# Optimization experiments

Hardware: AMD Instinct MI355X
Metric: run time of the kernel (lower is better)

## Reference

```python
import jax, jax.numpy as jnp
import numpy as np

B, P, K, D, T = 512, 64, 8, 512, 50000


def setup_inputs() -> dict:
    key = jax.random.key(0)
    k1, k2, k3, k4, k5, k6 = jax.random.split(key, 6)
    return {
        "inputs": jax.random.normal(k1, (B, P, D), dtype=jnp.float32),
        "title_emb_mat": jax.random.normal(k2, (T, D), dtype=jnp.float32),
        "nbr_batch": jax.random.randint(k3, (B, P, K), 0, B, dtype=jnp.int32),
        "nbr_job": jax.random.randint(k4, (B, P, K), 0, P, dtype=jnp.int32),
        "nbr_title": jax.random.randint(k5, (B, P, K), 0, T, dtype=jnp.int32),
        "nbr_mask": jax.random.randint(k6, (B, P, K), 0, 2, dtype=jnp.int32),
    }


def reference(inputs, title_emb_mat, nbr_batch, nbr_job, nbr_title, nbr_mask):
    # inputs:        [B, P, D]  job embeddings per employee position
    # title_emb_mat: [T, Dt]    title embedding table (Dt == D here)
    # nbr_*:         [B, P, K]  padded metapath neighbor indices + validity mask
    mask = nbr_mask.astype(bool)                              # [B,P,K]
    ref_embs = inputs[nbr_batch, nbr_job]                     # [B,P,K,D] gather of neighbor job embs
    # attention logits: focal emb vs neighbor embs (raw inner product, exp-normalized)
    raw_s = jnp.einsum('bpd,bpkd->bpk', inputs, ref_embs)     # [B,P,K]
    logits = jnp.where(mask, raw_s, jnp.float32(-1e9))
    sim = jax.nn.softmax(logits, axis=-1) * mask              # exact zeros on padded slots;
    # an all-masked (i,pos) -> uniform softmax * 0 mask == 0 row (matches torch 'continue' -> zeros)
    ref_t_embs = title_emb_mat[nbr_title]                     # [B,P,K,Dt] gather of target-title embs
    graph_concat = jnp.einsum('bpk,bpkt->bpt', sim, ref_t_embs)  # [B,P,Dt]
    out = jnp.concatenate([inputs, graph_concat], axis=-1)    # [B,P,D+Dt]
    return out.reshape(B * P, D + title_emb_mat.shape[1])     # torch.cat over batch, axis=0
```

## Files before the change

kernel.cpp:

```cpp
#include <hip/hip_runtime.h>

#define BB 512
#define PP 64
#define KK 8
#define DD 512

typedef float v4f __attribute__((ext_vector_type(4)));

__global__ __launch_bounds__(256, 2) void han_meta_kernel(
    const float* __restrict__ inputs,
    const float* __restrict__ title,
    const int*   __restrict__ nbr_batch,
    const int*   __restrict__ nbr_job,
    const int*   __restrict__ nbr_title,
    const int*   __restrict__ nbr_mask,
    float*       __restrict__ out)
{
    const int lane = threadIdx.x & 63;
    const int row = __builtin_amdgcn_readfirstlane(
        blockIdx.x * 4 + (threadIdx.x >> 6));

    const int* nb = nbr_batch + row * KK;
    const int* nj = nbr_job   + row * KK;
    const int* nt = nbr_title + row * KK;
    const int* nm = nbr_mask  + row * KK;
    int nbk[KK], njk[KK], ntk[KK], nmk[KK];
    #pragma unroll
    for (int k = 0; k < KK; ++k) {
        nbk[k] = __builtin_amdgcn_readfirstlane(nb[k]);
        njk[k] = __builtin_amdgcn_readfirstlane(nj[k]);
        ntk[k] = __builtin_amdgcn_readfirstlane(nt[k]);
        nmk[k] = __builtin_amdgcn_readfirstlane(nm[k]);
    }

    const unsigned focal_off = (unsigned)row * (DD * 4);
    unsigned goff[KK], toff[KK];
    #pragma unroll
    for (int k = 0; k < KK; ++k) {
        goff[k] = nmk[k] ? (unsigned)(nbk[k] * PP + njk[k]) * (DD * 4)
                         : focal_off;
        toff[k] = nmk[k] ? (unsigned)ntk[k] * (DD * 4)
                         : 0u;
    }

    const char* ibase = (const char*)inputs;
    const char* tbase = (const char*)title;
    const int lo = lane * 16;

    const float4 fa = *(const float4*)(ibase + focal_off + lo);
    const float4 fb = *(const float4*)(ibase + focal_off + lo + 1024);
    float4 ga[KK], gb[KK];
    #pragma unroll
    for (int k = 0; k < KK; ++k) {
        ga[k] = *(const float4*)(ibase + goff[k] + lo);
        gb[k] = *(const float4*)(ibase + goff[k] + lo + 1024);
    }
    float4 ta[KK], tb[KK];
    #pragma unroll
    for (int k = 0; k < KK; ++k) {
        ta[k] = *(const float4*)(tbase + toff[k] + lo);
        tb[k] = *(const float4*)(tbase + toff[k] + lo + 1024);
    }
    __builtin_amdgcn_sched_barrier(0);

    float d[KK];
    #pragma unroll
    for (int k = 0; k < KK; ++k) {
        d[k] = fa.x*ga[k].x + fa.y*ga[k].y + fa.z*ga[k].z + fa.w*ga[k].w
             + fb.x*gb[k].x + fb.y*gb[k].y + fb.z*gb[k].z + fb.w*gb[k].w;
    }

    #pragma unroll
    for (int off = 32; off >= 1; off >>= 1) {
        #pragma unroll
        for (int k = 0; k < KK; ++k)
            d[k] += __shfl_xor(d[k], off, 64);
    }

    float logit[KK];
    #pragma unroll
    for (int k = 0; k < KK; ++k) logit[k] = nmk[k] ? d[k] : -1e9f;
    float m = logit[0];
    #pragma unroll
    for (int k = 1; k < KK; ++k) m = fmaxf(m, logit[k]);
    float e[KK];
    float s = 0.0f;
    #pragma unroll
    for (int k = 0; k < KK; ++k) {
        e[k] = expf(logit[k] - m);
        s += e[k];
    }
    const float inv = 1.0f / s;
    float w[KK];
    #pragma unroll
    for (int k = 0; k < KK; ++k) w[k] = nmk[k] ? e[k] * inv : 0.0f;

    float4 oa = make_float4(0.f, 0.f, 0.f, 0.f);
    float4 ob = make_float4(0.f, 0.f, 0.f, 0.f);
    #pragma unroll
    for (int k = 0; k < KK; ++k) {
        oa.x += w[k]*ta[k].x; oa.y += w[k]*ta[k].y;
        oa.z += w[k]*ta[k].z; oa.w += w[k]*ta[k].w;
        ob.x += w[k]*tb[k].x; ob.y += w[k]*tb[k].y;
        ob.z += w[k]*tb[k].z; ob.w += w[k]*tb[k].w;
    }

    v4f* o4 = (v4f*)(out + (size_t)row * (2 * DD));
    v4f va = {fa.x, fa.y, fa.z, fa.w};
    v4f vb = {fb.x, fb.y, fb.z, fb.w};
    v4f vc = {oa.x, oa.y, oa.z, oa.w};
    v4f vd = {ob.x, ob.y, ob.z, ob.w};
    __builtin_nontemporal_store(va, o4 + lane);
    __builtin_nontemporal_store(vb, o4 + lane + 64);
    __builtin_nontemporal_store(vc, o4 + lane + 128);
    __builtin_nontemporal_store(vd, o4 + lane + 192);
}

extern "C" void kernel_launch(void* const* d_in, const int* in_sizes, int n_in,
                              void* d_out, int out_size, void* d_ws, size_t ws_size,
                              hipStream_t stream) {
    const float* inputs    = (const float*)d_in[0];
    const float* title     = (const float*)d_in[1];
    const int*   nbr_batch = (const int*)d_in[2];
    const int*   nbr_job   = (const int*)d_in[3];
    const int*   nbr_title = (const int*)d_in[4];
    const int*   nbr_mask  = (const int*)d_in[5];
    float*       out       = (float*)d_out;

    const int rows = BB * PP;
    dim3 grid(rows / 4);
    dim3 block(256);

    han_meta_kernel<<<grid, block, 0, stream>>>(
        inputs, title, nbr_batch, nbr_job, nbr_title, nbr_mask, out);
}
```

Baseline: 296.9 us.

## Stage neighbor and title gathers into LDS via async global_load_lds

The kernel now issues the 32 gathered row loads per output row as direct global-to-LDS transfers instead of loading into registers. It waits on partial vmcnt so the dot products can start while title rows are still in flight. Launches change to one 64-thread wave per block with 32KB of LDS each. The aim is to free VGPRs and raise memory-level parallelism. The 32KB LDS per block limits how many waves fit on a CU, and the vmcnt accounting depends on instruction ordering.

Result: slower. 318.6 us (+7.3%).

```diff
diff --git a/kernel.cpp b/kernel.cpp
--- a/kernel.cpp
+++ b/kernel.cpp
@@ -7,7 +7,15 @@
 
 typedef float v4f __attribute__((ext_vector_type(4)));
 
-__global__ __launch_bounds__(256, 2) void han_meta_kernel(
+
+__device__ __forceinline__ void async_1k(const void* g, void* l) {
+    __builtin_amdgcn_global_load_lds(
+        (const __attribute__((address_space(1))) void*)g,
+        (__attribute__((address_space(3))) void*)l,
+        16, 0, 0);
+}
+
+__global__ __launch_bounds__(64) void han_meta_kernel(
     const float* __restrict__ inputs,
     const float* __restrict__ title,
     const int*   __restrict__ nbr_batch,
@@ -16,9 +24,10 @@
     const int*   __restrict__ nbr_mask,
     float*       __restrict__ out)
 {
-    const int lane = threadIdx.x & 63;
-    const int row = __builtin_amdgcn_readfirstlane(
-        blockIdx.x * 4 + (threadIdx.x >> 6));
+    __shared__ float lds_f[8192];
+
+    const int lane = threadIdx.x;
+    const int row  = __builtin_amdgcn_readfirstlane(blockIdx.x);
 
     const int* nb = nbr_batch + row * KK;
     const int* nj = nbr_job   + row * KK;
@@ -45,29 +54,35 @@
 
     const char* ibase = (const char*)inputs;
     const char* tbase = (const char*)title;
-    const int lo = lane * 16;
+    char*       lbase = (char*)lds_f;
+    const unsigned lo = (unsigned)lane * 16;
+
+    #pragma unroll
+    for (int k = 0; k < KK; ++k) {
+        async_1k(ibase + goff[k] + lo,        lbase + k * 2048);
+        async_1k(ibase + goff[k] + lo + 1024, lbase + k * 2048 + 1024);
+    }
 
     const float4 fa = *(const float4*)(ibase + focal_off + lo);
     const float4 fb = *(const float4*)(ibase + focal_off + lo + 1024);
-    float4 ga[KK], gb[KK];
+
     #pragma unroll
     for (int k = 0; k < KK; ++k) {
-        ga[k] = *(const float4*)(ibase + goff[k] + lo);
-        gb[k] = *(const float4*)(ibase + goff[k] + lo + 1024);
+        async_1k(tbase + toff[k] + lo,        lbase + 16384 + k * 2048);
+        async_1k(tbase + toff[k] + lo + 1024, lbase + 16384 + k * 2048 + 1024);
     }
-    float4 ta[KK], tb[KK];
-    #pragma unroll
-    for (int k = 0; k < KK; ++k) {
-        ta[k] = *(const float4*)(tbase + toff[k] + lo);
-        tb[k] = *(const float4*)(tbase + toff[k] + lo + 1024);
-    }
+
+    asm volatile("s_waitcnt vmcnt(16)" ::: "memory");
     __builtin_amdgcn_sched_barrier(0);
 
+    const float4* l4 = (const float4*)lds_f;
     float d[KK];
     #pragma unroll
     for (int k = 0; k < KK; ++k) {
-        d[k] = fa.x*ga[k].x + fa.y*ga[k].y + fa.z*ga[k].z + fa.w*ga[k].w
-             + fb.x*gb[k].x + fb.y*gb[k].y + fb.z*gb[k].z + fb.w*gb[k].w;
+        const float4 ga = l4[k * 128 + lane];
+        const float4 gb = l4[k * 128 + 64 + lane];
+        d[k] = fa.x*ga.x + fa.y*ga.y + fa.z*ga.z + fa.w*ga.w
+             + fb.x*gb.x + fb.y*gb.y + fb.z*gb.z + fb.w*gb.w;
     }
 
     #pragma unroll
@@ -95,14 +110,17 @@
     #pragma unroll
     for (int k = 0; k < KK; ++k) w[k] = nmk[k] ? e[k] * inv : 0.0f;
 
+    asm volatile("s_waitcnt vmcnt(0)" ::: "memory");
+    __builtin_amdgcn_sched_barrier(0);
+
     float4 oa = make_float4(0.f, 0.f, 0.f, 0.f);
     float4 ob = make_float4(0.f, 0.f, 0.f, 0.f);
     #pragma unroll
     for (int k = 0; k < KK; ++k) {
-        oa.x += w[k]*ta[k].x; oa.y += w[k]*ta[k].y;
-        oa.z += w[k]*ta[k].z; oa.w += w[k]*ta[k].w;
-        ob.x += w[k]*tb[k].x; ob.y += w[k]*tb[k].y;
-        ob.z += w[k]*tb[k].z; ob.w += w[k]*tb[k].w;
+        const float4 ta = l4[1024 + k * 128 + lane];
+        const float4 tb = l4[1024 + k * 128 + 64 + lane];
+        oa.x += w[k]*ta.x; oa.y += w[k]*ta.y; oa.z += w[k]*ta.z; oa.w += w[k]*ta.w;
+        ob.x += w[k]*tb.x; ob.y += w[k]*tb.y; ob.z += w[k]*tb.z; ob.w += w[k]*tb.w;
     }
 
     v4f* o4 = (v4f*)(out + (size_t)row * (2 * DD));
@@ -128,8 +146,8 @@
     float*       out       = (float*)d_out;
 
     const int rows = BB * PP;
-    dim3 grid(rows / 4);
-    dim3 block(256);
+    dim3 grid(rows);
+    dim3 block(64);
 
     han_meta_kernel<<<grid, block, 0, stream>>>(
         inputs, title, nbr_batch, nbr_job, nbr_title, nbr_mask, out);
```
